# Kernel optimization log

Measured on AMD Instinct MI355X. Metric: run time of the kernel, lower is better.

Reference implementation:

```python
import jax, jax.numpy as jnp
import numpy as np

N_NODES = 50000
N_EDGES = 800000
D = 128           # 2 * hidden_channels
N_LAYERS = 9
N_GRAPHS = 256
EPS = 1e-05


def setup_inputs() -> dict:
    key = jax.random.key(0)
    ks = jax.random.split(key, 12)
    x = jax.random.normal(ks[0], (N_NODES, 13), dtype=jnp.float32)
    edge_index = jax.random.randint(ks[1], (2, N_EDGES), 0, N_NODES, dtype=jnp.int64)
    edge_attr = jax.random.normal(ks[2], (N_EDGES, 4), dtype=jnp.float32)
    batch = jnp.sort(jax.random.randint(ks[3], (N_NODES,), 0, N_GRAPHS, dtype=jnp.int64))
    s13 = 1.0 / np.sqrt(13)
    s4 = 1.0 / np.sqrt(4)
    sD = 1.0 / np.sqrt(D)
    s512 = 1.0 / np.sqrt(512)
    Wv = jax.random.uniform(ks[4], (13, D), jnp.float32, -s13, s13)
    We = jax.random.uniform(ks[5], (4, D), jnp.float32, -s4, s4)
    conv_w = jax.random.uniform(ks[6], (N_LAYERS, D, D), jnp.float32, -sD, sD)
    conv_b = jax.random.uniform(ks[7], (N_LAYERS, D), jnp.float32, -sD, sD)
    Wh1 = jax.random.uniform(ks[8], (D, 512), jnp.float32, -sD, sD)
    bh1 = jax.random.uniform(ks[9], (512,), jnp.float32, -sD, sD)
    Wh2 = jax.random.uniform(ks[10], (512, 1), jnp.float32, -s512, s512)
    bh2 = jax.random.uniform(ks[11], (1,), jnp.float32, -s512, s512)
    return {"x": x, "edge_index": edge_index, "edge_attr": edge_attr, "batch": batch,
            "Wv": Wv, "We": We, "conv_w": conv_w, "conv_b": conv_b,
            "Wh1": Wh1, "bh1": bh1, "Wh2": Wh2, "bh2": bh2}


def reference(x, edge_index, edge_attr, batch, Wv, We, conv_w, conv_b, Wh1, bh1, Wh2, bh2):
    src, dst = edge_index[0], edge_index[1]
    h = x @ Wv                      # [N, D]
    ea = edge_attr @ We             # [E, D]

    def layer(h, wb):
        W, b = wb
        msg = jax.nn.relu(h[src] + ea)                     # [E, D] gather + elementwise
        aggr = jax.ops.segment_sum(msg, dst, num_segments=N_NODES)  # scatter-add
        out = ((1.0 + EPS) * h + aggr) @ W + b             # GINEConv nn (Linear)
        return jax.nn.relu(out) + h, None                  # residual

    h, _ = jax.lax.scan(layer, h, (conv_w, conv_b))

    # global mean pool over graphs
    sums = jax.ops.segment_sum(h, batch, num_segments=N_GRAPHS)    # [G, D]
    cnt = jax.ops.segment_sum(jnp.ones((h.shape[0],), h.dtype), batch, num_segments=N_GRAPHS)
    pooled = sums / jnp.maximum(cnt, 1.0)[:, None]

    out = jax.nn.gelu(pooled @ Wh1 + bh1, approximate=False) @ Wh2 + bh2  # [G, 1]
    return out
```

## Files before the change

### kernel.cpp

```cpp
#include <hip/hip_runtime.h>
#include <math.h>

#define N_NODES 50000
#define N_EDGES 800000
#define DCH 128
#define N_LAYERS 9
#define N_GRAPHS 256
#define EPSF 1e-5f
#define NCHUNK 196
#define NSLICE 8
#define SL_SZ 6250

typedef __attribute__((ext_vector_type(8))) short short8;
typedef __attribute__((ext_vector_type(4))) float floatx4;

static __device__ __forceinline__ unsigned short f2bf(float f) {
    unsigned int u = __float_as_uint(f);
    unsigned int r = (u + 0x7fffu + ((u >> 16) & 1u)) >> 16;
    return (unsigned short)r;
}
static __device__ __forceinline__ unsigned int pack_bf2(float a, float b) {
    return (unsigned int)f2bf(a) | ((unsigned int)f2bf(b) << 16);
}
static __device__ __forceinline__ float bflo(unsigned int u) { return __uint_as_float(u << 16); }
static __device__ __forceinline__ float bfhi(unsigned int u) { return __uint_as_float(u & 0xffff0000u); }

static __device__ __forceinline__ float dot2bf(unsigned int a, unsigned int b, float c) {
    float d;
    asm("v_dot2_f32_bf16 %0, %1, %2, %3" : "=v"(d) : "v"(a), "v"(b), "v"(c));
    return d;
}

static __device__ __forceinline__ int dbucket(int d) { return 63 - min(d, 63); }

__global__ void hist_kernel(const int* __restrict__ dst, int* __restrict__ deg) {
    int t = blockIdx.x * 256 + threadIdx.x;
    atomicAdd(&deg[dst[t]], 1);
}

__global__ __launch_bounds__(256) void dsort_hist_kernel(const int* __restrict__ deg,
                                                         int* __restrict__ bhist) {
    __shared__ int lh[64];
    int t = threadIdx.x;
    if (t < 64) lh[t] = 0;
    __syncthreads();
    int n = blockIdx.x * 256 + t;
    if (n < N_NODES) atomicAdd(&lh[dbucket(deg[n])], 1);
    __syncthreads();
    if (t < 64) bhist[blockIdx.x * 64 + t] = lh[t];
}

__global__ __launch_bounds__(64) void dsort_scan_kernel(const int* __restrict__ bhist,
                                                        int* __restrict__ boff) {
    __shared__ int tot[64];
    __shared__ int base[64];
    int b = threadIdx.x;
    int s = 0;
    for (int blk = 0; blk < NCHUNK; blk++) s += bhist[blk * 64 + b];
    tot[b] = s;
    __syncthreads();
    if (b == 0) {
        int run = 0;
        for (int i = 0; i < 64; i++) { base[i] = run; run += tot[i]; }
    }
    __syncthreads();
    int run = base[b];
    for (int blk = 0; blk < NCHUNK; blk++) {
        boff[blk * 64 + b] = run;
        run += bhist[blk * 64 + b];
    }
}

__global__ __launch_bounds__(256) void dsort_scatter_kernel(const int* __restrict__ deg,
                                                            const int* __restrict__ boff,
                                                            int* __restrict__ nperm,
                                                            int* __restrict__ inv) {
    __shared__ int cur[64];
    int t = threadIdx.x;
    if (t < 64) cur[t] = boff[blockIdx.x * 64 + t];
    __syncthreads();
    int n = blockIdx.x * 256 + t;
    if (n < N_NODES) {
        int p = atomicAdd(&cur[dbucket(deg[n])], 1);
        nperm[p] = n;
        inv[n] = p;
    }
}

__global__ void dstinv_kernel(const int* __restrict__ dst, const int* __restrict__ inv,
                              int* __restrict__ dstinv) {
    int t = blockIdx.x * 256 + threadIdx.x;
    dstinv[t] = inv[dst[t]];
}

__global__ __launch_bounds__(256) void chunksum_kernel(const int* __restrict__ deg,
                                                       const int* __restrict__ nperm,
                                                       int* __restrict__ csum) {
    int t = threadIdx.x;
    int i = blockIdx.x * 256 + t;
    int v = (i < N_NODES) ? deg[nperm[i]] : 0;
    __shared__ int sh[4];
    for (int off = 32; off >= 1; off >>= 1) v += __shfl_down(v, off);
    if ((t & 63) == 0) sh[t >> 6] = v;
    __syncthreads();
    if (t == 0) csum[blockIdx.x] = sh[0] + sh[1] + sh[2] + sh[3];
}

__global__ __launch_bounds__(256) void chunkscan_kernel(const int* __restrict__ csum,
                                                        int* __restrict__ coff) {
    __shared__ int sh[256];
    int t = threadIdx.x;
    sh[t] = (t < NCHUNK) ? csum[t] : 0;
    __syncthreads();
    for (int off = 1; off < 256; off <<= 1) {
        int v = (t >= off) ? sh[t - off] : 0;
        __syncthreads();
        sh[t] += v;
        __syncthreads();
    }
    if (t < NCHUNK) coff[t] = t ? sh[t - 1] : 0;
}

__global__ __launch_bounds__(256) void applyscan_kernel(const int* __restrict__ deg,
                                                        const int* __restrict__ nperm,
                                                        const int* __restrict__ coff,
                                                        int* __restrict__ rowp,
                                                        int* __restrict__ cursor) {
    __shared__ int sh[256];
    int t = threadIdx.x;
    int i = blockIdx.x * 256 + t;
    int d = (i < N_NODES) ? deg[nperm[i]] : 0;
    sh[t] = d;
    __syncthreads();
    for (int off = 1; off < 256; off <<= 1) {
        int v = (t >= off) ? sh[t - off] : 0;
        __syncthreads();
        sh[t] += v;
        __syncthreads();
    }
    int excl = coff[blockIdx.x] + (t ? sh[t - 1] : 0);
    if (i < N_NODES) {
        rowp[i] = excl;
        cursor[i] = excl;
    }
    if (i == N_NODES - 1) rowp[N_NODES] = N_EDGES;
}

__global__ __launch_bounds__(256) void scatter_kernel(const int* __restrict__ src,
                                                      const int* __restrict__ dstinv,
                                                      const int* __restrict__ inv,
                                                      const float* __restrict__ eattr,
                                                      int* __restrict__ cursor,
                                                      uint4* __restrict__ erec) {
    int s = blockIdx.x & (NSLICE - 1);
    int chunk = blockIdx.x / NSLICE;
    int e0 = chunk * 1024 + threadIdx.x * 4;
    if (e0 >= N_EDGES) return;
    int4 d4 = *(const int4*)(dstinv + e0);
#pragma unroll
    for (int k = 0; k < 4; k++) {
        int e = e0 + k;
        int d = (k == 0) ? d4.x : (k == 1) ? d4.y : (k == 2) ? d4.z : d4.w;
        if (d / SL_SZ == s) {
            int p = atomicAdd(&cursor[d], 1);
            float4 a = ((const float4*)eattr)[e];
            erec[p] = make_uint4((unsigned int)inv[src[e]],
                                 pack_bf2(a.x, a.y), pack_bf2(a.z, a.w), 0u);
        }
    }
}

__global__ __launch_bounds__(256) void wconv_kernel(const float* __restrict__ convW,
                                                    uint4* __restrict__ wb) {
    int tid = blockIdx.x * 256 + threadIdx.x;
    int lane = tid & 63;
    int t = (tid >> 6) & 31;
    int layer = tid >> 11;
    int jt = t >> 2, kt = t & 3;
    int quad = lane >> 4, col = lane & 15;
    const float* Wl = convW + (size_t)layer * DCH * DCH;
    int kbase = kt * 32 + quad * 8;
    int ch = jt * 16 + col;
    unsigned int d0 = pack_bf2(Wl[(kbase + 0) * DCH + ch], Wl[(kbase + 1) * DCH + ch]);
    unsigned int d1 = pack_bf2(Wl[(kbase + 2) * DCH + ch], Wl[(kbase + 3) * DCH + ch]);
    unsigned int d2 = pack_bf2(Wl[(kbase + 4) * DCH + ch], Wl[(kbase + 5) * DCH + ch]);
    unsigned int d3 = pack_bf2(Wl[(kbase + 6) * DCH + ch], Wl[(kbase + 7) * DCH + ch]);
    wb[tid] = make_uint4(d0, d1, d2, d3);
}

__global__ void h0_kernel(const float* __restrict__ x, const float* __restrict__ Wv,
                          const int* __restrict__ inv,
                          unsigned int* __restrict__ hbf) {
    int t = blockIdx.x * 256 + threadIdx.x;
    int n = t >> 6, l = t & 63;
    const float* xr = x + n * 13;
    float s0 = 0.f, s1 = 0.f;
#pragma unroll
    for (int j = 0; j < 13; j++) {
        float xv = xr[j];
        s0 = fmaf(xv, Wv[j * 128 + 2 * l], s0);
        s1 = fmaf(xv, Wv[j * 128 + 2 * l + 1], s1);
    }
    int p = inv[n];
    hbf[(size_t)p * 64 + l] = pack_bf2(s0, s1);
}

#define VSTRIDE 68
#define OLP 132
__global__ __launch_bounds__(256) void layer_kernel(const unsigned int* __restrict__ hbfA,
                                                    const uint4* __restrict__ erec,
                                                    const int* __restrict__ rowp,
                                                    const float* __restrict__ We,
                                                    const short8* __restrict__ wbL,
                                                    const float* __restrict__ b,
                                                    unsigned int* __restrict__ hbfB) {
    __shared__ unsigned int vsh[16 * VSTRIDE];
    __shared__ float ol[16 * OLP];
    __shared__ unsigned int hsh[16 * 64];
    int tid = threadIdx.x;
    int lane = tid & 63;
    int wave = tid >> 6;
    int nb = blockIdx.x * 16;
    unsigned int wy0 = pack_bf2(We[0 * 128 + 2 * lane], We[1 * 128 + 2 * lane]);
    unsigned int wz0 = pack_bf2(We[2 * 128 + 2 * lane], We[3 * 128 + 2 * lane]);
    unsigned int wy1 = pack_bf2(We[0 * 128 + 2 * lane + 1], We[1 * 128 + 2 * lane + 1]);
    unsigned int wz1 = pack_bf2(We[2 * 128 + 2 * lane + 1], We[3 * 128 + 2 * lane + 1]);

    int n0 = nb + wave * 4;
    int s0 = __builtin_amdgcn_readfirstlane(rowp[n0]);
    int s1 = __builtin_amdgcn_readfirstlane(rowp[n0 + 1]);
    int s2 = __builtin_amdgcn_readfirstlane(rowp[n0 + 2]);
    int s3 = __builtin_amdgcn_readfirstlane(rowp[n0 + 3]);
    int s4 = __builtin_amdgcn_readfirstlane(rowp[n0 + 4]);
    int d0 = s1 - s0, d1 = s2 - s1, d2 = s3 - s2, d3 = s4 - s3;
    int dm0 = d0 - 1, dm1 = d1 - 1, dm2 = d2 - 1, dm3 = d3 - 1;
    int maxd = max(max(d0, d1), max(d2, d3));
    int mm = maxd - 1;

    unsigned int hn0 = hbfA[(size_t)(n0 + 0) * 64 + lane];
    unsigned int hn1 = hbfA[(size_t)(n0 + 1) * 64 + lane];
    unsigned int hn2 = hbfA[(size_t)(n0 + 2) * 64 + lane];
    unsigned int hn3 = hbfA[(size_t)(n0 + 3) * 64 + lane];
    hsh[(wave * 4 + 0) * 64 + lane] = hn0;
    hsh[(wave * 4 + 1) * 64 + lane] = hn1;
    hsh[(wave * 4 + 2) * 64 + lane] = hn2;
    hsh[(wave * 4 + 3) * 64 + lane] = hn3;

    float c0x = 0.f, c0y = 0.f, c1x = 0.f, c1y = 0.f;
    float c2x = 0.f, c2y = 0.f, c3x = 0.f, c3y = 0.f;

    if (maxd > 0) {
        uint4 qa0 = erec[s0 + min(0, dm0)];
        uint4 qa1 = erec[s1 + min(0, dm1)];
        uint4 qa2 = erec[s2 + min(0, dm2)];
        uint4 qa3 = erec[s3 + min(0, dm3)];
        int i1 = min(1, mm);
        uint4 qb0 = erec[s0 + min(i1, dm0)];
        uint4 qb1 = erec[s1 + min(i1, dm1)];
        uint4 qb2 = erec[s2 + min(i1, dm2)];
        uint4 qb3 = erec[s3 + min(i1, dm3)];
        for (int i = 0; i < maxd; i += 2) {
            unsigned int ua0 = hbfA[qa0.x * 64u + (unsigned)lane];
            unsigned int ua1 = hbfA[qa1.x * 64u + (unsigned)lane];
            unsigned int ua2 = hbfA[qa2.x * 64u + (unsigned)lane];
            unsigned int ua3 = hbfA[qa3.x * 64u + (unsigned)lane];
            unsigned int ub0 = hbfA[qb0.x * 64u + (unsigned)lane];
            unsigned int ub1 = hbfA[qb1.x * 64u + (unsigned)lane];
            unsigned int ub2 = hbfA[qb2.x * 64u + (unsigned)lane];
            unsigned int ub3 = hbfA[qb3.x * 64u + (unsigned)lane];
            unsigned int ya0 = qa0.y, za0 = qa0.z, ya1 = qa1.y, za1 = qa1.z;
            unsigned int ya2 = qa2.y, za2 = qa2.z, ya3 = qa3.y, za3 = qa3.z;
            unsigned int yb0 = qb0.y, zb0 = qb0.z, yb1 = qb1.y, zb1 = qb1.z;
            unsigned int yb2 = qb2.y, zb2 = qb2.z, yb3 = qb3.y, zb3 = qb3.z;
            int i2 = min(i + 2, mm);
            int i3 = min(i + 3, mm);
            qa0 = erec[s0 + min(i2, dm0)];
            qa1 = erec[s1 + min(i2, dm1)];
            qa2 = erec[s2 + min(i2, dm2)];
            qa3 = erec[s3 + min(i2, dm3)];
            qb0 = erec[s0 + min(i3, dm0)];
            qb1 = erec[s1 + min(i3, dm1)];
            qb2 = erec[s2 + min(i3, dm2)];
            qb3 = erec[s3 + min(i3, dm3)];
            float ma00 = dot2bf(ya0, wy0, dot2bf(za0, wz0, 0.f));
            float ma01 = dot2bf(ya0, wy1, dot2bf(za0, wz1, 0.f));
            float ma10 = dot2bf(ya1, wy0, dot2bf(za1, wz0, 0.f));
            float ma11 = dot2bf(ya1, wy1, dot2bf(za1, wz1, 0.f));
            float ma20 = dot2bf(ya2, wy0, dot2bf(za2, wz0, 0.f));
            float ma21 = dot2bf(ya2, wy1, dot2bf(za2, wz1, 0.f));
            float ma30 = dot2bf(ya3, wy0, dot2bf(za3, wz0, 0.f));
            float ma31 = dot2bf(ya3, wy1, dot2bf(za3, wz1, 0.f));
            c0x += (i < d0) ? fmaxf(bflo(ua0) + ma00, 0.f) : 0.f;
            c0y += (i < d0) ? fmaxf(bfhi(ua0) + ma01, 0.f) : 0.f;
            c1x += (i < d1) ? fmaxf(bflo(ua1) + ma10, 0.f) : 0.f;
            c1y += (i < d1) ? fmaxf(bfhi(ua1) + ma11, 0.f) : 0.f;
            c2x += (i < d2) ? fmaxf(bflo(ua2) + ma20, 0.f) : 0.f;
            c2y += (i < d2) ? fmaxf(bfhi(ua2) + ma21, 0.f) : 0.f;
            c3x += (i < d3) ? fmaxf(bflo(ua3) + ma30, 0.f) : 0.f;
            c3y += (i < d3) ? fmaxf(bfhi(ua3) + ma31, 0.f) : 0.f;
            float mb00 = dot2bf(yb0, wy0, dot2bf(zb0, wz0, 0.f));
            float mb01 = dot2bf(yb0, wy1, dot2bf(zb0, wz1, 0.f));
            float mb10 = dot2bf(yb1, wy0, dot2bf(zb1, wz0, 0.f));
            float mb11 = dot2bf(yb1, wy1, dot2bf(zb1, wz1, 0.f));
            float mb20 = dot2bf(yb2, wy0, dot2bf(zb2, wz0, 0.f));
            float mb21 = dot2bf(yb2, wy1, dot2bf(zb2, wz1, 0.f));
            float mb30 = dot2bf(yb3, wy0, dot2bf(zb3, wz0, 0.f));
            float mb31 = dot2bf(yb3, wy1, dot2bf(zb3, wz1, 0.f));
            int ip = i + 1;
            c0x += (ip < d0) ? fmaxf(bflo(ub0) + mb00, 0.f) : 0.f;
            c0y += (ip < d0) ? fmaxf(bfhi(ub0) + mb01, 0.f) : 0.f;
            c1x += (ip < d1) ? fmaxf(bflo(ub1) + mb10, 0.f) : 0.f;
            c1y += (ip < d1) ? fmaxf(bfhi(ub1) + mb11, 0.f) : 0.f;
            c2x += (ip < d2) ? fmaxf(bflo(ub2) + mb20, 0.f) : 0.f;
            c2y += (ip < d2) ? fmaxf(bfhi(ub2) + mb21, 0.f) : 0.f;
            c3x += (ip < d3) ? fmaxf(bflo(ub3) + mb30, 0.f) : 0.f;
            c3y += (ip < d3) ? fmaxf(bfhi(ub3) + mb31, 0.f) : 0.f;
        }
    }
    vsh[(wave * 4 + 0) * VSTRIDE + lane] =
        pack_bf2(fmaf(bflo(hn0), 1.f + EPSF, c0x), fmaf(bfhi(hn0), 1.f + EPSF, c0y));
    vsh[(wave * 4 + 1) * VSTRIDE + lane] =
        pack_bf2(fmaf(bflo(hn1), 1.f + EPSF, c1x), fmaf(bfhi(hn1), 1.f + EPSF, c1y));
    vsh[(wave * 4 + 2) * VSTRIDE + lane] =
        pack_bf2(fmaf(bflo(hn2), 1.f + EPSF, c2x), fmaf(bfhi(hn2), 1.f + EPSF, c2y));
    vsh[(wave * 4 + 3) * VSTRIDE + lane] =
        pack_bf2(fmaf(bflo(hn3), 1.f + EPSF, c3x), fmaf(bfhi(hn3), 1.f + EPSF, c3y));

    __syncthreads();
    int col = lane & 15, quad = lane >> 4;
    short8 a[4];
#pragma unroll
    for (int kt = 0; kt < 4; kt++) {
        a[kt] = *(const short8*)(vsh + col * VSTRIDE + kt * 16 + quad * 4);
    }
#pragma unroll
    for (int jj = 0; jj < 2; jj++) {
        int jt = wave * 2 + jj;
        floatx4 acc = {0.f, 0.f, 0.f, 0.f};
#pragma unroll
        for (int kt = 0; kt < 4; kt++) {
            short8 bf = wbL[(jt * 4 + kt) * 64 + lane];
            acc = __builtin_amdgcn_mfma_f32_16x16x32_bf16(a[kt], bf, acc, 0, 0, 0);
        }
        float bv = b[jt * 16 + col];
#pragma unroll
        for (int r = 0; r < 4; r++) {
            ol[(quad * 4 + r) * OLP + jt * 16 + col] = fmaxf(acc[r] + bv, 0.f);
        }
    }
    __syncthreads();
    uint2* b2v = (uint2*)hbfB;
#pragma unroll
    for (int i = 0; i < 2; i++) {
        int idx = i * 256 + tid;
        int nl2 = idx >> 5, c4 = idx & 31;
        int node = nb + nl2;
        const float* row = ol + nl2 * OLP + c4 * 4;
        unsigned int h01 = hsh[nl2 * 64 + 2 * c4];
        unsigned int h23 = hsh[nl2 * 64 + 2 * c4 + 1];
        float r0 = row[0] + bflo(h01);
        float r1 = row[1] + bfhi(h01);
        float r2 = row[2] + bflo(h23);
        float r3 = row[3] + bfhi(h23);
        b2v[(size_t)node * 32 + c4] = make_uint2(pack_bf2(r0, r1), pack_bf2(r2, r3));
    }
}

__global__ void bounds_kernel(const int* __restrict__ batch, int* __restrict__ gs) {
    int n = blockIdx.x * 256 + threadIdx.x;
    if (n >= N_NODES) return;
    int bcur = batch[n];
    int prev = (n == 0) ? -1 : batch[n - 1];
    for (int g = prev + 1; g <= bcur; g++) gs[g] = n;
    if (n == N_NODES - 1) {
        for (int g = bcur + 1; g <= N_GRAPHS; g++) gs[g] = N_NODES;
    }
}

__global__ __launch_bounds__(256) void pool_kernel(const unsigned int* __restrict__ hbf,
                                                   const int* __restrict__ inv,
                                                   const int* __restrict__ batch,
                                                   float* __restrict__ sums) {
    int wave = threadIdx.x >> 6, l = threadIdx.x & 63;
    int nbase = (blockIdx.x * 4 + wave) * 8;
    float a0 = 0.f, a1 = 0.f;
    int g = -1;
#pragma unroll
    for (int i = 0; i < 8; i++) {
        int n = nbase + i;
        if (n >= N_NODES) break;
        int bg = batch[n];
        if (bg != g) {
            if (g >= 0) {
                atomicAdd(&sums[g * 128 + 2 * l], a0);
                atomicAdd(&sums[g * 128 + 2 * l + 1], a1);
            }
            g = bg; a0 = 0.f; a1 = 0.f;
        }
        int p = inv[n];
        unsigned int hv = hbf[(size_t)p * 64 + l];
        a0 += bflo(hv); a1 += bfhi(hv);
    }
    if (g >= 0) {
        atomicAdd(&sums[g * 128 + 2 * l], a0);
        atomicAdd(&sums[g * 128 + 2 * l + 1], a1);
    }
}

__global__ __launch_bounds__(512) void mlp_kernel(const float* __restrict__ sums,
                                                  const int* __restrict__ gs,
                                                  const float* __restrict__ Wh1,
                                                  const float* __restrict__ bh1,
                                                  const float* __restrict__ Wh2,
                                                  const float* __restrict__ bh2,
                                                  float* __restrict__ out) {
    int g = blockIdx.x;
    __shared__ float pl[128];
    __shared__ float red[8];
    int tid = threadIdx.x;
    if (tid < 128) {
        float cnt = fmaxf((float)(gs[g + 1] - gs[g]), 1.0f);
        pl[tid] = sums[g * 128 + tid] / cnt;
    }
    __syncthreads();
    float s = bh1[tid];
#pragma unroll 16
    for (int k = 0; k < 128; k++) s = fmaf(pl[k], Wh1[k * 512 + tid], s);
    float gl = 0.5f * s * (1.0f + erff(s * 0.70710678118654752f));
    float p = gl * Wh2[tid];
    for (int off = 32; off >= 1; off >>= 1) p += __shfl_down(p, off);
    if ((tid & 63) == 0) red[tid >> 6] = p;
    __syncthreads();
    if (tid == 0) {
        float tot = 0.f;
        for (int i = 0; i < 8; i++) tot += red[i];
        out[g] = tot + bh2[0];
    }
}

extern "C" void kernel_launch(void* const* d_in, const int* in_sizes, int n_in,
                              void* d_out, int out_size, void* d_ws, size_t ws_size,
                              hipStream_t stream) {
    const float* x = (const float*)d_in[0];
    const int* ei = (const int*)d_in[1];
    const float* eattr = (const float*)d_in[2];
    const int* batch = (const int*)d_in[3];
    const float* Wv = (const float*)d_in[4];
    const float* We = (const float*)d_in[5];
    const float* convW = (const float*)d_in[6];
    const float* convB = (const float*)d_in[7];
    const float* Wh1 = (const float*)d_in[8];
    const float* bh1 = (const float*)d_in[9];
    const float* Wh2 = (const float*)d_in[10];
    const float* bh2 = (const float*)d_in[11];
    float* out = (float*)d_out;

    const int* src = ei;
    const int* dst = ei + N_EDGES;

    char* w = (char*)d_ws;
    size_t off = 0;
    auto alloc = [&](size_t bytes) -> char* {
        char* p = w + off;
        off += (bytes + 255) & ~(size_t)255;
        return p;
    };
    unsigned int* hbfA = (unsigned int*)alloc((size_t)N_NODES * 64 * 4);
    unsigned int* hbfB = (unsigned int*)alloc((size_t)N_NODES * 64 * 4);
    uint4* wb = (uint4*)alloc((size_t)N_LAYERS * 32 * 64 * 16);
    int* deg = (int*)alloc((size_t)(N_NODES + 1) * 4);
    int* rowp = (int*)alloc((size_t)(N_NODES + 1) * 4);
    int* cursor = (int*)alloc((size_t)(N_NODES + 1) * 4);
    int* csum = (int*)alloc((size_t)NCHUNK * 4);
    int* coff = (int*)alloc((size_t)NCHUNK * 4);
    int* bhist = (int*)alloc((size_t)NCHUNK * 64 * 4);
    int* boff = (int*)alloc((size_t)NCHUNK * 64 * 4);
    int* nperm = (int*)alloc((size_t)N_NODES * 4);
    int* inv = (int*)alloc((size_t)N_NODES * 4);
    int* dstinv = (int*)alloc((size_t)N_EDGES * 4);
    uint4* erec = (uint4*)alloc((size_t)N_EDGES * 16);
    int* gs = (int*)alloc((size_t)(N_GRAPHS + 1) * 4);
    float* sums = (float*)alloc((size_t)N_GRAPHS * DCH * 4);
    (void)ws_size; (void)n_in; (void)in_sizes; (void)out_size;

    hipMemsetAsync(deg, 0, (size_t)(N_NODES + 1) * 4, stream);
    hipMemsetAsync(sums, 0, (size_t)N_GRAPHS * DCH * 4, stream);

    hist_kernel<<<N_EDGES / 256, 256, 0, stream>>>(dst, deg);
    dsort_hist_kernel<<<NCHUNK, 256, 0, stream>>>(deg, bhist);
    dsort_scan_kernel<<<1, 64, 0, stream>>>(bhist, boff);
    dsort_scatter_kernel<<<NCHUNK, 256, 0, stream>>>(deg, boff, nperm, inv);
    dstinv_kernel<<<N_EDGES / 256, 256, 0, stream>>>(dst, inv, dstinv);
    chunksum_kernel<<<NCHUNK, 256, 0, stream>>>(deg, nperm, csum);
    chunkscan_kernel<<<1, 256, 0, stream>>>(csum, coff);
    applyscan_kernel<<<NCHUNK, 256, 0, stream>>>(deg, nperm, coff, rowp, cursor);
    scatter_kernel<<<782 * NSLICE, 256, 0, stream>>>(src, dstinv, inv, eattr, cursor, erec);
    wconv_kernel<<<72, 256, 0, stream>>>(convW, wb);
    h0_kernel<<<N_NODES * 64 / 256, 256, 0, stream>>>(x, Wv, inv, hbfA);
    bounds_kernel<<<(N_NODES + 255) / 256, 256, 0, stream>>>(batch, gs);

    unsigned int* bfcur = hbfA;
    unsigned int* bfnext = hbfB;
    for (int layer = 0; layer < N_LAYERS; layer++) {
        layer_kernel<<<N_NODES / 16, 256, 0, stream>>>(
            bfcur, erec, rowp, We,
            (const short8*)(wb + (size_t)layer * 2048), convB + (size_t)layer * DCH,
            bfnext);
        unsigned int* tb = bfcur; bfcur = bfnext; bfnext = tb;
    }

    pool_kernel<<<(N_NODES + 31) / 32, 256, 0, stream>>>(bfcur, inv, batch, sums);
    mlp_kernel<<<N_GRAPHS, 512, 0, stream>>>(sums, gs, Wh1, bh1, Wh2, bh2, out);
}
```

Before: 572.8 us.

## Replace sliced CSR scatter with two-pass bucket partition of edge records

Drops the dstinv pass and the 8-way sliced scatter, which reread the destination array 8 times. In their place, a partition kernel builds full edge records and appends them to 16 destination-range buckets using block-local counts and one global atomic per bucket. A bucket kernel then scatters each bucket into CSR order through per-node cursor atomics, so writes within a slice stay localized. It adds a large intermediate buffer of 16x131072 records and assumes no bucket exceeds that capacity, which only holds for roughly uniform destinations.

```diff
diff --git a/kernel.cpp b/kernel.cpp
--- a/kernel.cpp
+++ b/kernel.cpp
@@ -8,8 +8,9 @@
 #define N_GRAPHS 256
 #define EPSF 1e-5f
 #define NCHUNK 196
-#define NSLICE 8
-#define SL_SZ 6250
+#define NSLICE16 16
+#define SL16 3125
+#define BUCKET_CAP 131072
 
 typedef __attribute__((ext_vector_type(8))) short short8;
 typedef __attribute__((ext_vector_type(4))) float floatx4;
@@ -85,12 +86,6 @@
         nperm[p] = n;
         inv[n] = p;
     }
-}
-
-__global__ void dstinv_kernel(const int* __restrict__ dst, const int* __restrict__ inv,
-                              int* __restrict__ dstinv) {
-    int t = blockIdx.x * 256 + threadIdx.x;
-    dstinv[t] = inv[dst[t]];
 }
 
 __global__ __launch_bounds__(256) void chunksum_kernel(const int* __restrict__ deg,
@@ -146,26 +141,62 @@
     if (i == N_NODES - 1) rowp[N_NODES] = N_EDGES;
 }
 
-__global__ __launch_bounds__(256) void scatter_kernel(const int* __restrict__ src,
-                                                      const int* __restrict__ dstinv,
-                                                      const int* __restrict__ inv,
-                                                      const float* __restrict__ eattr,
-                                                      int* __restrict__ cursor,
-                                                      uint4* __restrict__ erec) {
-    int s = blockIdx.x & (NSLICE - 1);
-    int chunk = blockIdx.x / NSLICE;
-    int e0 = chunk * 1024 + threadIdx.x * 4;
-    if (e0 >= N_EDGES) return;
-    int4 d4 = *(const int4*)(dstinv + e0);
+__global__ __launch_bounds__(256) void partition_kernel(const int* __restrict__ src,
+                                                        const int* __restrict__ dst,
+                                                        const int* __restrict__ inv,
+                                                        const float* __restrict__ eattr,
+                                                        int* __restrict__ tails,
+                                                        uint4* __restrict__ buckets) {
+    __shared__ int cnt[NSLICE16];
+    __shared__ int base[NSLICE16];
+    int t = threadIdx.x;
+    if (t < NSLICE16) cnt[t] = 0;
+    __syncthreads();
+    int e0 = blockIdx.x * 1024 + t * 4;
+    uint4 rec[4];
+    int sl[4], slot[4];
+    int nv = 0;
 #pragma unroll
     for (int k = 0; k < 4; k++) {
         int e = e0 + k;
-        int d = (k == 0) ? d4.x : (k == 1) ? d4.y : (k == 2) ? d4.z : d4.w;
-        if (d / SL_SZ == s) {
+        if (e < N_EDGES) {
+            int d = inv[dst[e]];
+            int s = inv[src[e]];
+            float4 a = ((const float4*)eattr)[e];
+            int sli = d / SL16;
+            rec[k] = make_uint4((unsigned int)s, pack_bf2(a.x, a.y), pack_bf2(a.z, a.w),
+                                (unsigned int)d);
+            sl[k] = sli;
+            slot[k] = atomicAdd(&cnt[sli], 1);
+            nv = k + 1;
+        }
+    }
+    __syncthreads();
+    if (t < NSLICE16) base[t] = (cnt[t] > 0) ? atomicAdd(&tails[t], cnt[t]) : 0;
+    __syncthreads();
+    for (int k = 0; k < nv; k++) {
+        buckets[(size_t)sl[k] * BUCKET_CAP + base[sl[k]] + slot[k]] = rec[k];
+    }
+}
+
+__global__ __launch_bounds__(256) void bucket_kernel(const int* __restrict__ tails,
+                                                     const uint4* __restrict__ buckets,
+                                                     int* __restrict__ cursor,
+                                                     uint4* __restrict__ erec) {
+    int s = blockIdx.x & (NSLICE16 - 1);
+    int j = blockIdx.x >> 4;
+    int tl = tails[s];
+    int r0 = j * 1024 + threadIdx.x * 4;
+    if (r0 >= tl) return;
+    const uint4* bk = buckets + (size_t)s * BUCKET_CAP;
+#pragma unroll
+    for (int k = 0; k < 4; k++) {
+        int r = r0 + k;
+        if (r < tl) {
+            uint4 rec = bk[r];
+            int d = (int)rec.w;
             int p = atomicAdd(&cursor[d], 1);
-            float4 a = ((const float4*)eattr)[e];
-            erec[p] = make_uint4((unsigned int)inv[src[e]],
-                                 pack_bf2(a.x, a.y), pack_bf2(a.z, a.w), 0u);
+            erec[p] = rec;
         }
     }
 }
@@ -477,24 +508,28 @@
     int* boff = (int*)alloc((size_t)NCHUNK * 64 * 4);
     int* nperm = (int*)alloc((size_t)N_NODES * 4);
     int* inv = (int*)alloc((size_t)N_NODES * 4);
-    int* dstinv = (int*)alloc((size_t)N_EDGES * 4);
+    int* tails = (int*)alloc((size_t)NSLICE16 * 4);
+    uint4* buckets = (uint4*)alloc((size_t)NSLICE16 * BUCKET_CAP * 16);
     uint4* erec = (uint4*)alloc((size_t)N_EDGES * 16);
     int* gs = (int*)alloc((size_t)(N_GRAPHS + 1) * 4);
     float* sums = (float*)alloc((size_t)N_GRAPHS * DCH * 4);
     (void)ws_size; (void)n_in; (void)in_sizes; (void)out_size;
 
     hipMemsetAsync(deg, 0, (size_t)(N_NODES + 1) * 4, stream);
+    hipMemsetAsync(tails, 0, (size_t)NSLICE16 * 4, stream);
     hipMemsetAsync(sums, 0, (size_t)N_GRAPHS * DCH * 4, stream);
 
     hist_kernel<<<N_EDGES / 256, 256, 0, stream>>>(dst, deg);
     dsort_hist_kernel<<<NCHUNK, 256, 0, stream>>>(deg, bhist);
     dsort_scan_kernel<<<1, 64, 0, stream>>>(bhist, boff);
     dsort_scatter_kernel<<<NCHUNK, 256, 0, stream>>>(deg, boff, nperm, inv);
-    dstinv_kernel<<<N_EDGES / 256, 256, 0, stream>>>(dst, inv, dstinv);
     chunksum_kernel<<<NCHUNK, 256, 0, stream>>>(deg, nperm, csum);
     chunkscan_kernel<<<1, 256, 0, stream>>>(csum, coff);
     applyscan_kernel<<<NCHUNK, 256, 0, stream>>>(deg, nperm, coff, rowp, cursor);
-    scatter_kernel<<<782 * NSLICE, 256, 0, stream>>>(src, dstinv, inv, eattr, cursor, erec);
+    partition_kernel<<<(N_EDGES + 1023) / 1024, 256, 0, stream>>>(src, dst, inv, eattr,
+                                                                  tails, buckets);
+    bucket_kernel<<<(BUCKET_CAP / 1024) * NSLICE16, 256, 0, stream>>>(tails, buckets,
+                                                                      cursor, erec);
     wconv_kernel<<<72, 256, 0, stream>>>(convW, wb);
     h0_kernel<<<N_NODES * 64 / 256, 256, 0, stream>>>(x, Wv, inv, hbfA);
     bounds_kernel<<<(N_NODES + 255) / 256, 256, 0, stream>>>(batch, gs);
```

Result: no change. 583.1 us (+1.8%).
